# Kernel optimization log

Measured on AMD Instinct MI355X. Metric: run time of the kernel, lower is better.

## Reference

```python
import jax, jax.numpy as jnp
import numpy as np
import math


def setup_inputs() -> dict:
    key = jax.random.key(0)
    ks = jax.random.split(key, 5)
    B, L, H = 16384, 336, 168
    T = L + H
    T_air = jax.random.normal(ks[0], (B, T), dtype=jnp.float32) * 8.0 + 10.0
    T_obs = T_air + jax.random.normal(ks[1], (B, T), dtype=jnp.float32) * 2.0
    wind = jax.random.uniform(ks[2], (B, T), dtype=jnp.float32) * 10.0
    par = jax.random.uniform(ks[3], (B, T), dtype=jnp.float32) * 500.0
    dt = jax.random.uniform(ks[4], (B, T), dtype=jnp.float32) * 3600.0 + 1800.0
    k_init = 1e-4
    k_raw = jnp.float32(k_init + math.log(-math.expm1(-k_init)))  # softplus inverse
    return {
        "T_obs": T_obs, "T_air": T_air, "wind": wind, "par": par, "dt": dt,
        "L_hist": L,
        "k_raw": k_raw,
        "log_q": jnp.float32(-8.0), "log_r": jnp.float32(-4.0),
        "log_p0": jnp.float32(-2.0), "log_q_scale": jnp.float32(0.0),
        "theta_par_lin": jnp.float32(1e-5), "theta_par_quad": jnp.float32(1e-8),
        "theta_wind_cool": jnp.float32(-1e-5), "theta_sensible": jnp.float32(-1e-6),
        "theta_forced_conv": jnp.float32(-1e-7),
    }


def reference(T_obs, T_air, wind, par, dt, L_hist, k_raw, log_q, log_r, log_p0,
              log_q_scale, theta_par_lin, theta_par_quad, theta_wind_cool,
              theta_sensible, theta_forced_conv):
    B, T_total = T_obs.shape
    L = int(L_hist)
    H = T_total - L

    k = jax.nn.softplus(k_raw)
    q = jnp.exp(log_q)
    q_scale = jnp.exp(log_q_scale)
    R = jnp.exp(log_r)
    P0 = jnp.exp(log_p0)

    def predict(T, P, Ta, w, p, dtt):
        dT = T - Ta
        cl = (theta_par_lin * p + theta_par_quad * p * p + theta_wind_cool * w
              + theta_sensible * dT + theta_forced_conv * w * dT)
        T_pred = jnp.clip(T - k * dT * dtt + cl * dtt, -50.0, 100.0)
        F = jnp.clip(1.0 - k * dtt + (theta_sensible + theta_forced_conv * w) * dtt, -2.0, 2.0)
        P_pred = jnp.clip(F * F * P + q_scale * q * dtt, 1e-10, 1e6)
        return T_pred, P_pred

    def filt_step(carry, xs):
        T, P = carry
        Ta, w, p, dtt, y = xs
        Tp, Pp = predict(T, P, Ta, w, p, dtt)
        S = Pp + R
        K = Pp / S
        T_upd = Tp + K * (y - Tp)
        P_upd = (1.0 - K) ** 2 * Pp + K * K * R
        return (T_upd, P_upd), None

    s0 = T_obs[:, 0]
    P0b = jnp.broadcast_to(P0, (B,)).astype(T_obs.dtype)

    # filtering over t = 1 .. L-1 (forcing from t-1, dt/obs at t)
    filt_xs = (T_air[:, :L - 1].T, wind[:, :L - 1].T, par[:, :L - 1].T,
               jnp.clip(dt[:, 1:L], 1.0, None).T, T_obs[:, 1:L].T)
    (s, P), _ = jax.lax.scan(filt_step, (s0, P0b), filt_xs)

    def fcst_step(carry, xs):
        T, P = carry
        Ta, w, p, dtt = xs
        Tp, Pp = predict(T, P, Ta, w, p, dtt)
        return (Tp, Pp), (Tp, Pp)

    # open-loop forecast over t = L .. L+H-1 (forcing from idx-1)
    fcst_xs = (T_air[:, L - 1:L + H - 1].T, wind[:, L - 1:L + H - 1].T,
               par[:, L - 1:L + H - 1].T, jnp.clip(dt[:, L:], 1.0, None).T)
    _, (T_preds, T_vars) = jax.lax.scan(fcst_step, (s, P), fcst_xs)

    return T_preds.T, T_vars.T  # each [B, H]
```

## Files before the change

### kernel.cpp

```cpp
#include <hip/hip_runtime.h>

namespace {
constexpr int kB = 16384;
constexpr int kL = 336;
constexpr int kH = 168;
constexpr int kT = 504;
constexpr int kW = 16;
constexpr int kNW = 32;
constexpr int kFiltW = 21;
constexpr int kRS = 65;
constexpr int kTile = kW * kRS;
constexpr int kORS = 17;
constexpr int kOTile = 64 * kORS;
constexpr int oA  = 0;
constexpr int oWd = oA  + 2 * kTile;
constexpr int oP  = oWd + 2 * kTile;
constexpr int oD  = oP  + 2 * kTile;
constexpr int oY  = oD  + 2 * kTile;
constexpr int oOT = oY  + 2 * kTile;
constexpr int oOV = oOT + 2 * kOTile;
constexpr int kLdsWords = oOV + 2 * kOTile;
}

__global__ __launch_bounds__(256, 1)
void kf_kernel(const float* __restrict__ g_obs,
               const float* __restrict__ g_air,
               const float* __restrict__ g_wind,
               const float* __restrict__ g_par,
               const float* __restrict__ g_dt,
               const float* __restrict__ s_k_raw,
               const float* __restrict__ s_log_q,
               const float* __restrict__ s_log_r,
               const float* __restrict__ s_log_p0,
               const float* __restrict__ s_log_qs,
               const float* __restrict__ s_th_pl,
               const float* __restrict__ s_th_pq,
               const float* __restrict__ s_th_wc,
               const float* __restrict__ s_th_s,
               const float* __restrict__ s_th_fc,
               float* __restrict__ out)
{
    __shared__ float lds[kLdsWords];
    const int tid  = threadIdx.x;
    const int wid  = tid >> 6;
    const int lane = tid & 63;
    const int r0   = blockIdx.x * 64;

    auto stage = [&](const float* __restrict__ g, int basew, int buf, int wn) {
        const int t0 = wn * kW;
        const int tb = basew + buf * kTile;
#pragma unroll
        for (int kk = 0; kk < 4; ++kk) {
            const int flat = kk * 64 + lane;
            const int row = flat >> 2, q = flat & 3;
            int tq = t0 + q * 4;
            tq = tq > 500 ? 500 : tq;
            const float4 v = *(const float4*)(g + (size_t)(r0 + row) * kT + tq);
            const int wb = tb + row + (q * 4) * kRS;
            lds[wb          ] = v.x;
            lds[wb +     kRS] = v.y;
            lds[wb + 2 * kRS] = v.z;
            lds[wb + 3 * kRS] = v.w;
        }
    };

    float* outT = out;
    float* outV = out + (size_t)kB * kH;

    auto store_out = [&](int wn) {
        const int buf = wn & 1;
        const int h0 = wn * kW - kL;
#pragma unroll
        for (int kk = 0; kk < 4; ++kk) {
            const int flat = kk * 64 + lane;
            const int row = flat >> 2, q = flat & 3;
            const int h = h0 + q * 4;
            if (h + 3 < kH) {
                const int rb = oOT + buf * kOTile + row * kORS + q * 4;
                const int vb = oOV + buf * kOTile + row * kORS + q * 4;
                float4 tv, vv;
                tv.x = lds[rb]; tv.y = lds[rb + 1]; tv.z = lds[rb + 2]; tv.w = lds[rb + 3];
                vv.x = lds[vb]; vv.y = lds[vb + 1]; vv.z = lds[vb + 2]; vv.w = lds[vb + 3];
                *(float4*)(outT + (size_t)(r0 + row) * kH + h) = tv;
                *(float4*)(outV + (size_t)(r0 + row) * kH + h) = vv;
            }
        }
    };

    float kpar = 0, qq = 0, R = 0, P = 0, Tst = 0;
    float th_pl = 0, th_pq = 0, th_wc = 0, th_s = 0, th_fc = 0;
    float aC = 0, wC = 0, pC = 0;

    if (wid == 0) {
        kpar = log1pf(expf(s_k_raw[0]));
        qq   = expf(s_log_q[0]) * expf(s_log_qs[0]);
        R    = expf(s_log_r[0]);
        P    = expf(s_log_p0[0]);
        th_pl = s_th_pl[0]; th_pq = s_th_pq[0]; th_wc = s_th_wc[0];
        th_s  = s_th_s[0];  th_fc = s_th_fc[0];
    } else if (wid == 1) {
        stage(g_air, oA, 0, 0); stage(g_wind, oWd, 0, 0);
    } else if (wid == 2) {
        stage(g_par, oP, 0, 0); stage(g_dt, oD, 0, 0);
    } else {
        stage(g_obs, oY, 0, 0);
    }
    __syncthreads();

    for (int w = 0; w < kNW; ++w) {
        const int buf = w & 1;
        if (wid == 0) {
            const int Ab = oA  + buf * kTile, Wb = oWd + buf * kTile;
            const int Pb = oP  + buf * kTile, Db = oD  + buf * kTile;
            const int Yb = oY  + buf * kTile;
            int trel = 0;
            if (w == 0) {
                Tst = lds[Yb + lane];
                aC = lds[Ab + lane]; wC = lds[Wb + lane]; pC = lds[Pb + lane];
                trel = 1;
            }
            if (w < kFiltW) {
                for (; trel < kW; ++trel) {
                    const float D = lds[Db + trel * kRS + lane];
                    const float Y = lds[Yb + trel * kRS + lane];
                    const float dtt = fmaxf(D, 1.0f);
                    const float dT = Tst - aC;
                    const float gk = fmaf(th_fc, wC, th_s) - kpar;
                    const float base = fmaf(pC, fmaf(th_pq, pC, th_pl), th_wc * wC);
                    const float Tp = fminf(fmaxf(fmaf(fmaf(gk, dT, base), dtt, Tst), -50.0f), 100.0f);
                    const float F = fminf(fmaxf(fmaf(gk, dtt, 1.0f), -2.0f), 2.0f);
                    const float Pp = fminf(fmaxf(fmaf(F * F, P, qq * dtt), 1e-10f), 1e6f);
                    const float Kg = Pp * __builtin_amdgcn_rcpf(Pp + R);
                    Tst = fmaf(Kg, Y - Tp, Tp);
                    const float omk = 1.0f - Kg;
                    P = fmaf(omk * omk, Pp, Kg * Kg * R);
                    aC = lds[Ab + trel * kRS + lane];
                    wC = lds[Wb + trel * kRS + lane];
                    pC = lds[Pb + trel * kRS + lane];
                }
            } else {
                const int tmax = (w == kNW - 1) ? 8 : kW;
                const int ob = oOT + buf * kOTile + lane * kORS;
                const int vb = oOV + buf * kOTile + lane * kORS;
                for (; trel < tmax; ++trel) {
                    const float D = lds[Db + trel * kRS + lane];
                    const float dtt = fmaxf(D, 1.0f);
                    const float dT = Tst - aC;
                    const float gk = fmaf(th_fc, wC, th_s) - kpar;
                    const float base = fmaf(pC, fmaf(th_pq, pC, th_pl), th_wc * wC);
                    Tst = fminf(fmaxf(fmaf(fmaf(gk, dT, base), dtt, Tst), -50.0f), 100.0f);
                    const float F = fminf(fmaxf(fmaf(gk, dtt, 1.0f), -2.0f), 2.0f);
                    P = fminf(fmaxf(fmaf(F * F, P, qq * dtt), 1e-10f), 1e6f);
                    lds[ob + trel] = Tst;
                    lds[vb + trel] = P;
                    aC = lds[Ab + trel * kRS + lane];
                    wC = lds[Wb + trel * kRS + lane];
                    pC = lds[Pb + trel * kRS + lane];
                }
            }
        } else if (wid == 1) {
            if (w + 1 < kNW) { stage(g_air, oA, (w + 1) & 1, w + 1);
                               stage(g_wind, oWd, (w + 1) & 1, w + 1); }
        } else if (wid == 2) {
            if (w + 1 < kNW) { stage(g_par, oP, (w + 1) & 1, w + 1);
                               stage(g_dt, oD, (w + 1) & 1, w + 1); }
        } else {
            if (w + 1 < kFiltW) stage(g_obs, oY, (w + 1) & 1, w + 1);
            if (w - 1 >= kFiltW) store_out(w - 1);
        }
        __syncthreads();
    }
    if (wid == 3) store_out(kNW - 1);
}

extern "C" void kernel_launch(void* const* d_in, const int* in_sizes, int n_in,
                              void* d_out, int out_size, void* d_ws, size_t ws_size,
                              hipStream_t stream) {
    const float* g_obs  = (const float*)d_in[0];
    const float* g_air  = (const float*)d_in[1];
    const float* g_wind = (const float*)d_in[2];
    const float* g_par  = (const float*)d_in[3];
    const float* g_dt   = (const float*)d_in[4];
    const float* k_raw  = (const float*)d_in[6];
    const float* log_q  = (const float*)d_in[7];
    const float* log_r  = (const float*)d_in[8];
    const float* log_p0 = (const float*)d_in[9];
    const float* log_qs = (const float*)d_in[10];
    const float* th_pl  = (const float*)d_in[11];
    const float* th_pq  = (const float*)d_in[12];
    const float* th_wc  = (const float*)d_in[13];
    const float* th_s   = (const float*)d_in[14];
    const float* th_fc  = (const float*)d_in[15];
    float* out = (float*)d_out;

    dim3 grid(kB / 64), block(256);
    hipLaunchKernelGGL(kf_kernel, grid, block, 0, stream,
                       g_obs, g_air, g_wind, g_par, g_dt,
                       k_raw, log_q, log_r, log_p0, log_qs,
                       th_pl, th_pq, th_wc, th_s, th_fc, out);
}
```

Measured before the change: 220.7 us.

## Pre-transpose inputs to time-major fp16 workspace and scan with register pipelining

Adds a pre-pass kernel that transposes the five input streams into time-major, 8-step fp16-packed chunks in workspace. A new single-wave scan kernel then reads one coalesced uint4 per stream per chunk and keeps four chunks of loads in flight in registers, replacing the LDS-staged producer/consumer warps. This aims to hide global load latency in the serial recurrence, at the cost of an extra full read/write pass and reduced input precision from fp16 storage. The old kernel remains as a fallback when workspace is too small.

```diff
diff --git a/kernel.cpp b/kernel.cpp
--- a/kernel.cpp
+++ b/kernel.cpp
@@ -1,10 +1,219 @@
 #include <hip/hip_runtime.h>
+#include <hip/hip_fp16.h>
 
 namespace {
 constexpr int kB = 16384;
 constexpr int kL = 336;
 constexpr int kH = 168;
 constexpr int kT = 504;
+constexpr int kC8 = 63;
+constexpr int kFiltC8 = 42;
+constexpr size_t kStreamU4 = (size_t)kC8 * kB;
+constexpr size_t kWsNeed = (4 * (size_t)kC8 + 42) * (size_t)kB * 16;
+}
+
+__global__ __launch_bounds__(256)
+void xpose_kernel(const float* __restrict__ g_obs,
+                  const float* __restrict__ g_air,
+                  const float* __restrict__ g_wind,
+                  const float* __restrict__ g_par,
+                  const float* __restrict__ g_dt,
+                  uint4* __restrict__ ws4)
+{
+    extern __shared__ float tile[];
+    const int tid = threadIdx.x, wid = tid >> 6, lane = tid & 63;
+    const int r0 = blockIdx.x * 64;
+    const int tb = blockIdx.y;
+    const int s  = blockIdx.z;
+    const float* src = s == 0 ? g_air : s == 1 ? g_wind : s == 2 ? g_par
+                     : s == 3 ? g_dt  : g_obs;
+    uint4* dst = ws4 + (size_t)s * kStreamU4;
+    const int t0 = tb * 248;
+
+#pragma unroll
+    for (int it = 0; it < 16; ++it) {
+        const int r = it * 4 + wid;
+        const float4 v = *(const float4*)(src + (size_t)(r0 + r) * kT + t0 + lane * 4);
+        *(float4*)&tile[r * 260 + lane * 4] = v;
+    }
+    __syncthreads();
+
+    const int cbase = tb * 31;
+#pragma unroll
+    for (int it = 0; it < 8; ++it) {
+        const int cl = it * 4 + wid;
+        const int c8 = cbase + cl;
+        if (s == 4 && c8 >= kFiltC8) continue;
+        const float* rp = &tile[lane * 260 + cl * 8];
+        const float4 f0 = *(const float4*)(rp);
+        const float4 f1 = *(const float4*)(rp + 4);
+        union { __half2 h; unsigned u; } c0, c1, c2, c3;
+        c0.h = __floats2half2_rn(f0.x, f0.y);
+        c1.h = __floats2half2_rn(f0.z, f0.w);
+        c2.h = __floats2half2_rn(f1.x, f1.y);
+        c3.h = __floats2half2_rn(f1.z, f1.w);
+        uint4 u; u.x = c0.u; u.y = c1.u; u.z = c2.u; u.w = c3.u;
+        dst[(size_t)c8 * kB + r0 + lane] = u;
+    }
+}
+
+__device__ inline void up2(unsigned u, float& a, float& b) {
+    union { unsigned u; __half2 h; } cv; cv.u = u;
+    const float2 f = __half22float2(cv.h);
+    a = f.x; b = f.y;
+}
+__device__ inline void up8(uint4 u, float* v) {
+    up2(u.x, v[0], v[1]); up2(u.y, v[2], v[3]);
+    up2(u.z, v[4], v[5]); up2(u.w, v[6], v[7]);
+}
+
+struct Qc { uint4 a, w, p, d, y; };
+
+__global__ __launch_bounds__(64, 1)
+void kf_scan_x(const uint4* __restrict__ X,
+               const float* __restrict__ s_k_raw,
+               const float* __restrict__ s_log_q,
+               const float* __restrict__ s_log_r,
+               const float* __restrict__ s_log_p0,
+               const float* __restrict__ s_log_qs,
+               const float* __restrict__ s_th_pl,
+               const float* __restrict__ s_th_pq,
+               const float* __restrict__ s_th_wc,
+               const float* __restrict__ s_th_s,
+               const float* __restrict__ s_th_fc,
+               float* __restrict__ out)
+{
+    extern __shared__ float lt[];
+    float* ldsT = lt;
+    float* ldsV = lt + 64 * 172;
+    const int lane = threadIdx.x;
+    const int b0 = blockIdx.x * 64;
+
+    const uint4* XA = X;
+    const uint4* XW = X + kStreamU4;
+    const uint4* XP = X + 2 * kStreamU4;
+    const uint4* XD = X + 3 * kStreamU4;
+    const uint4* XY = X + 4 * kStreamU4;
+
+    const float kpar = log1pf(expf(s_k_raw[0]));
+    const float qq   = expf(s_log_q[0]) * expf(s_log_qs[0]);
+    const float R    = expf(s_log_r[0]);
+    float P          = expf(s_log_p0[0]);
+    const float th_pl = s_th_pl[0], th_pq = s_th_pq[0], th_wc = s_th_wc[0];
+    const float th_s  = s_th_s[0],  th_fc = s_th_fc[0];
+
+    float Tst = 0.0f, aC = 0.0f, wC = 0.0f, pC = 0.0f;
+
+    auto load = [&](Qc& q, int c) {
+        const int nc = c < kC8 ? c : kC8 - 1;
+        const size_t off = (size_t)nc * kB + b0 + lane;
+        q.a = XA[off]; q.w = XW[off]; q.p = XP[off]; q.d = XD[off];
+        const int yc = nc < kFiltC8 ? nc : kFiltC8 - 1;
+        q.y = XY[(size_t)yc * kB + b0 + lane];
+        __builtin_amdgcn_sched_barrier(0);
+    };
+
+    auto kstep = [&](float Ta, float w, float p, float draw, float y) {
+        const float dtt = fmaxf(draw, 1.0f);
+        const float dT = Tst - Ta;
+        const float gk = fmaf(th_fc, w, th_s) - kpar;
+        const float base = fmaf(p, fmaf(th_pq, p, th_pl), th_wc * w);
+        const float Tp = fminf(fmaxf(fmaf(fmaf(gk, dT, base), dtt, Tst), -50.0f), 100.0f);
+        const float F = fminf(fmaxf(fmaf(gk, dtt, 1.0f), -2.0f), 2.0f);
+        const float Pp = fminf(fmaxf(fmaf(F * F, P, qq * dtt), 1e-10f), 1e6f);
+        const float Kg = Pp * __builtin_amdgcn_rcpf(Pp + R);
+        Tst = fmaf(Kg, y - Tp, Tp);
+        const float omk = 1.0f - Kg;
+        P = fmaf(omk * omk, Pp, Kg * Kg * R);
+    };
+    auto fstep = [&](float Ta, float w, float p, float draw) {
+        const float dtt = fmaxf(draw, 1.0f);
+        const float dT = Tst - Ta;
+        const float gk = fmaf(th_fc, w, th_s) - kpar;
+        const float base = fmaf(p, fmaf(th_pq, p, th_pl), th_wc * w);
+        Tst = fminf(fmaxf(fmaf(fmaf(gk, dT, base), dtt, Tst), -50.0f), 100.0f);
+        const float F = fminf(fmaxf(fmaf(gk, dtt, 1.0f), -2.0f), 2.0f);
+        P = fminf(fmaxf(fmaf(F * F, P, qq * dtt), 1e-10f), 1e6f);
+    };
+
+    auto cK = [&](const Qc& q) {
+        float A[8], W[8], Pr[8], D[8], Y[8];
+        up8(q.a, A); up8(q.w, W); up8(q.p, Pr); up8(q.d, D); up8(q.y, Y);
+        kstep(aC, wC, pC, D[0], Y[0]);
+#pragma unroll
+        for (int j = 1; j < 8; ++j) kstep(A[j-1], W[j-1], Pr[j-1], D[j], Y[j]);
+        aC = A[7]; wC = W[7]; pC = Pr[7];
+    };
+
+    auto cF = [&](const Qc& q, int c) {
+        float A[8], W[8], Pr[8], D[8], oT[8], oV[8];
+        up8(q.a, A); up8(q.w, W); up8(q.p, Pr); up8(q.d, D);
+        fstep(aC, wC, pC, D[0]); oT[0] = Tst; oV[0] = P;
+#pragma unroll
+        for (int j = 1; j < 8; ++j) {
+            fstep(A[j-1], W[j-1], Pr[j-1], D[j]);
+            oT[j] = Tst; oV[j] = P;
+        }
+        aC = A[7]; wC = W[7]; pC = Pr[7];
+        const int h0 = (c - kFiltC8) * 8;
+        *(float4*)&ldsT[lane * 172 + h0    ] = make_float4(oT[0], oT[1], oT[2], oT[3]);
+        *(float4*)&ldsT[lane * 172 + h0 + 4] = make_float4(oT[4], oT[5], oT[6], oT[7]);
+        *(float4*)&ldsV[lane * 172 + h0    ] = make_float4(oV[0], oV[1], oV[2], oV[3]);
+        *(float4*)&ldsV[lane * 172 + h0 + 4] = make_float4(oV[4], oV[5], oV[6], oV[7]);
+    };
+
+    Qc q0, q1, q2, q3;
+    load(q0, 0); load(q1, 1); load(q2, 2); load(q3, 3);
+
+    {
+        float A[8], W[8], Pr[8], D[8], Y[8];
+        up8(q0.a, A); up8(q0.w, W); up8(q0.p, Pr); up8(q0.d, D); up8(q0.y, Y);
+        Tst = Y[0];
+        aC = A[0]; wC = W[0]; pC = Pr[0];
+#pragma unroll
+        for (int j = 1; j < 8; ++j) kstep(A[j-1], W[j-1], Pr[j-1], D[j], Y[j]);
+        aC = A[7]; wC = W[7]; pC = Pr[7];
+    }
+    load(q0, 4);
+    cK(q1); load(q1, 5);
+    cK(q2); load(q2, 6);
+    cK(q3); load(q3, 7);
+
+#pragma unroll 1
+    for (int g = 0; g < 9; ++g) {
+        const int base = 4 * g + 4;
+        cK(q0); load(q0, base + 4);
+        cK(q1); load(q1, base + 5);
+        cK(q2); load(q2, base + 6);
+        cK(q3); load(q3, base + 7);
+    }
+    cK(q0); load(q0, 44);
+    cK(q1); load(q1, 45);
+
+#pragma unroll 1
+    for (int g = 0; g < 5; ++g) {
+        const int base = kFiltC8 + 4 * g;
+        cF(q2, base + 0); load(q2, base + 4);
+        cF(q3, base + 1); load(q3, base + 5);
+        cF(q0, base + 2); load(q0, base + 6);
+        cF(q1, base + 3); load(q1, base + 7);
+    }
+    cF(q2, 62);
+
+    float* outT = out;
+    float* outV = out + (size_t)kB * kH;
+#pragma unroll 1
+    for (int r = 0; r < 64; ++r) {
+        if (lane < 42) {
+            const float4 tv = *(const float4*)&ldsT[r * 172 + lane * 4];
+            const float4 vv = *(const float4*)&ldsV[r * 172 + lane * 4];
+            *(float4*)(outT + (size_t)(b0 + r) * kH + lane * 4) = tv;
+            *(float4*)(outV + (size_t)(b0 + r) * kH + lane * 4) = vv;
+        }
+    }
+}
+
+namespace fb {
 constexpr int kW = 16;
 constexpr int kNW = 32;
 constexpr int kFiltW = 21;
@@ -40,6 +249,7 @@
                const float* __restrict__ s_th_fc,
                float* __restrict__ out)
 {
+    using namespace fb;
     __shared__ float lds[kLdsWords];
     const int tid  = threadIdx.x;
     const int wid  = tid >> 6;
@@ -193,9 +403,21 @@
     const float* th_fc  = (const float*)d_in[15];
     float* out = (float*)d_out;
 
-    dim3 grid(kB / 64), block(256);
-    hipLaunchKernelGGL(kf_kernel, grid, block, 0, stream,
-                       g_obs, g_air, g_wind, g_par, g_dt,
-                       k_raw, log_q, log_r, log_p0, log_qs,
-                       th_pl, th_pq, th_wc, th_s, th_fc, out);
-}
+    if (ws_size >= kWsNeed) {
+        uint4* ws4 = (uint4*)d_ws;
+        dim3 xg(kB / 64, 2, 5), xb(256);
+        hipLaunchKernelGGL(xpose_kernel, xg, xb, 64 * 260 * 4, stream,
+                           g_obs, g_air, g_wind, g_par, g_dt, ws4);
+        dim3 sg(kB / 64), sb(64);
+        hipLaunchKernelGGL(kf_scan_x, sg, sb, 2 * 64 * 172 * 4, stream,
+                           (const uint4*)ws4,
+                           k_raw, log_q, log_r, log_p0, log_qs,
+                           th_pl, th_pq, th_wc, th_s, th_fc, out);
+    } else {
+        dim3 grid(kB / 64), block(256);
+        hipLaunchKernelGGL(kf_kernel, grid, block, 0, stream,
+                           g_obs, g_air, g_wind, g_par, g_dt,
+                           k_raw, log_q, log_r, log_p0, log_qs,
+                           th_pl, th_pq, th_wc, th_s, th_fc, out);
+    }
+}
```

New measurement: 246.5 us. +11.7%, slower.

## Replace block barriers with LDS flag producer-consumer sync and fp16 input staging

Applied to the files above, without the earlier changes.

Removes the per-window __syncthreads that forces the compute wave to wait on loader waves. Loader and compute waves now hand off double-buffered tiles through atomic counters in LDS with sleep-polling. Inputs (air, wind, par, dt, obs) are also converted to fp16 in LDS to halve LDS footprint and traffic. Global loads change from float4 row chunks to scalar loads. The fp16 conversion loses precision: dt up to 5400 and par up to 500 have coarse fp16 spacing, which risks tolerance failures. The polling loop breaks out after a bounded number of spins, which risks a silent race.

```diff
diff --git a/kernel.cpp b/kernel.cpp
--- a/kernel.cpp
+++ b/kernel.cpp
@@ -1,4 +1,5 @@
 #include <hip/hip_runtime.h>
+#include <hip/hip_fp16.h>
 
 namespace {
 constexpr int kB = 16384;
@@ -7,170 +8,198 @@
 constexpr int kT = 504;
 constexpr int kW = 16;
 constexpr int kNW = 32;
-constexpr int kFiltW = 21;
-constexpr int kRS = 65;
-constexpr int kTile = kW * kRS;
-constexpr int kORS = 17;
-constexpr int kOTile = 64 * kORS;
-constexpr int oA  = 0;
-constexpr int oWd = oA  + 2 * kTile;
-constexpr int oP  = oWd + 2 * kTile;
-constexpr int oD  = oP  + 2 * kTile;
-constexpr int oY  = oD  + 2 * kTile;
-constexpr int oOT = oY  + 2 * kTile;
-constexpr int oOV = oOT + 2 * kOTile;
-constexpr int kLdsWords = oOV + 2 * kOTile;
+constexpr int kFW = 21;
+constexpr int kIS = 66;
+constexpr int kITile = kW * kIS;
+constexpr int kOS = 17;
+constexpr int kOTile = 64 * kOS;
+}
+
+__device__ inline void fwait(int* f, int target) {
+    int guard = 0;
+    while (__hip_atomic_load(f, __ATOMIC_ACQUIRE, __HIP_MEMORY_SCOPE_WORKGROUP) < target) {
+        __builtin_amdgcn_s_sleep(1);
+        if (++guard > (1 << 22)) break;
+    }
+}
+__device__ inline void fpost(int* f, int lane) {
+    __threadfence_block();
+    if (lane == 0) atomicAdd(f, 1);
 }
 
 __global__ __launch_bounds__(256, 1)
-void kf_kernel(const float* __restrict__ g_obs,
-               const float* __restrict__ g_air,
-               const float* __restrict__ g_wind,
-               const float* __restrict__ g_par,
-               const float* __restrict__ g_dt,
-               const float* __restrict__ s_k_raw,
-               const float* __restrict__ s_log_q,
-               const float* __restrict__ s_log_r,
-               const float* __restrict__ s_log_p0,
-               const float* __restrict__ s_log_qs,
-               const float* __restrict__ s_th_pl,
-               const float* __restrict__ s_th_pq,
-               const float* __restrict__ s_th_wc,
-               const float* __restrict__ s_th_s,
-               const float* __restrict__ s_th_fc,
-               float* __restrict__ out)
+void kf_fused(const float* __restrict__ g_obs,
+              const float* __restrict__ g_air,
+              const float* __restrict__ g_wind,
+              const float* __restrict__ g_par,
+              const float* __restrict__ g_dt,
+              const float* __restrict__ s_k_raw,
+              const float* __restrict__ s_log_q,
+              const float* __restrict__ s_log_r,
+              const float* __restrict__ s_log_p0,
+              const float* __restrict__ s_log_qs,
+              const float* __restrict__ s_th_pl,
+              const float* __restrict__ s_th_pq,
+              const float* __restrict__ s_th_wc,
+              const float* __restrict__ s_th_s,
+              const float* __restrict__ s_th_fc,
+              float* __restrict__ out)
 {
-    __shared__ float lds[kLdsWords];
-    const int tid  = threadIdx.x;
-    const int wid  = tid >> 6;
-    const int lane = tid & 63;
-    const int r0   = blockIdx.x * 64;
-
-    auto stage = [&](const float* __restrict__ g, int basew, int buf, int wn) {
-        const int t0 = wn * kW;
-        const int tb = basew + buf * kTile;
-#pragma unroll
-        for (int kk = 0; kk < 4; ++kk) {
-            const int flat = kk * 64 + lane;
-            const int row = flat >> 2, q = flat & 3;
-            int tq = t0 + q * 4;
-            tq = tq > 500 ? 500 : tq;
-            const float4 v = *(const float4*)(g + (size_t)(r0 + row) * kT + tq);
-            const int wb = tb + row + (q * 4) * kRS;
-            lds[wb          ] = v.x;
-            lds[wb +     kRS] = v.y;
-            lds[wb + 2 * kRS] = v.z;
-            lds[wb + 3 * kRS] = v.w;
-        }
-    };
-
-    float* outT = out;
-    float* outV = out + (size_t)kB * kH;
-
-    auto store_out = [&](int wn) {
-        const int buf = wn & 1;
-        const int h0 = wn * kW - kL;
-#pragma unroll
-        for (int kk = 0; kk < 4; ++kk) {
-            const int flat = kk * 64 + lane;
-            const int row = flat >> 2, q = flat & 3;
-            const int h = h0 + q * 4;
-            if (h + 3 < kH) {
-                const int rb = oOT + buf * kOTile + row * kORS + q * 4;
-                const int vb = oOV + buf * kOTile + row * kORS + q * 4;
-                float4 tv, vv;
-                tv.x = lds[rb]; tv.y = lds[rb + 1]; tv.z = lds[rb + 2]; tv.w = lds[rb + 3];
-                vv.x = lds[vb]; vv.y = lds[vb + 1]; vv.z = lds[vb + 2]; vv.w = lds[vb + 3];
-                *(float4*)(outT + (size_t)(r0 + row) * kH + h) = tv;
-                *(float4*)(outV + (size_t)(r0 + row) * kH + h) = vv;
-            }
-        }
-    };
-
-    float kpar = 0, qq = 0, R = 0, P = 0, Tst = 0;
-    float th_pl = 0, th_pq = 0, th_wc = 0, th_s = 0, th_fc = 0;
-    float aC = 0, wC = 0, pC = 0;
-
-    if (wid == 0) {
-        kpar = log1pf(expf(s_k_raw[0]));
-        qq   = expf(s_log_q[0]) * expf(s_log_qs[0]);
-        R    = expf(s_log_r[0]);
-        P    = expf(s_log_p0[0]);
-        th_pl = s_th_pl[0]; th_pq = s_th_pq[0]; th_wc = s_th_wc[0];
-        th_s  = s_th_s[0];  th_fc = s_th_fc[0];
-    } else if (wid == 1) {
-        stage(g_air, oA, 0, 0); stage(g_wind, oWd, 0, 0);
-    } else if (wid == 2) {
-        stage(g_par, oP, 0, 0); stage(g_dt, oD, 0, 0);
+    __shared__ __half s_in[5][2][kITile];
+    __shared__ float  s_oT[2][kOTile];
+    __shared__ float  s_oV[2][kOTile];
+    __shared__ int    s_flag[8];
+
+    const int tid = threadIdx.x, wid = tid >> 6, lane = tid & 63;
+    const int b0 = blockIdx.x * 64;
+
+    if (tid < 8) s_flag[tid] = 0;
+    __syncthreads();
+
+    int* pcAW = &s_flag[0];
+    int* pcPD = &s_flag[1];
+    int* pcY  = &s_flag[2];
+    int* cc   = &s_flag[3];
+    int* sc   = &s_flag[4];
+
+    if (wid == 1 || wid == 2) {
+        const float* g0 = (wid == 1) ? g_air  : g_par;
+        const float* g1 = (wid == 1) ? g_wind : g_dt;
+        __half* base0 = (wid == 1) ? &s_in[0][0][0] : &s_in[2][0][0];
+        __half* base1 = (wid == 1) ? &s_in[1][0][0] : &s_in[3][0][0];
+        int* pc = (wid == 1) ? pcAW : pcPD;
+        const int rloc = lane >> 4, trel = lane & 15;
+        for (int w = 0; w < kNW; ++w) {
+            if (w >= 2) fwait(cc, w - 1);
+            const int bi = w & 1;
+            int t = w * kW + trel; if (t > kT - 1) t = kT - 1;
+            float v0[16], v1[16];
+#pragma unroll
+            for (int i = 0; i < 16; ++i) {
+                const size_t off = (size_t)(b0 + 4 * i + rloc) * kT + t;
+                v0[i] = g0[off];
+                v1[i] = g1[off];
+            }
+            __half* d0 = base0 + bi * kITile;
+            __half* d1 = base1 + bi * kITile;
+#pragma unroll
+            for (int i = 0; i < 16; ++i) {
+                const int idx = trel * kIS + 4 * i + rloc;
+                d0[idx] = __float2half(v0[i]);
+                d1[idx] = __float2half(v1[i]);
+            }
+            fpost(pc, lane);
+        }
+    } else if (wid == 3) {
+        const int rloc = lane >> 4, trel = lane & 15;
+        for (int w = 0; w < kFW; ++w) {
+            if (w >= 2) fwait(cc, w - 1);
+            const int bi = w & 1;
+            const int t = w * kW + trel;
+            float v[16];
+#pragma unroll
+            for (int i = 0; i < 16; ++i)
+                v[i] = g_obs[(size_t)(b0 + 4 * i + rloc) * kT + t];
+            __half* d = &s_in[4][bi][0];
+#pragma unroll
+            for (int i = 0; i < 16; ++i)
+                d[trel * kIS + 4 * i + rloc] = __float2half(v[i]);
+            fpost(pcY, lane);
+        }
+        const int rq = lane & 3, rr = lane >> 2;
+        float* outT = out;
+        float* outV = out + (size_t)kB * kH;
+        for (int w = kFW; w < kNW; ++w) {
+            fwait(cc, w + 1);
+            const int bi = w & 1;
+            const int h0 = (w - kFW) * kW;
+            const int nq = (w == kNW - 1) ? 2 : 4;
+#pragma unroll
+            for (int i = 0; i < 4; ++i) {
+                const int r = 16 * i + rr;
+                if (rq < nq) {
+                    const float4 tv = *(const float4*)&s_oT[bi][r * kOS + rq * 4];
+                    const float4 vv = *(const float4*)&s_oV[bi][r * kOS + rq * 4];
+                    *(float4*)&outT[(size_t)(b0 + r) * kH + h0 + rq * 4] = tv;
+                    *(float4*)&outV[(size_t)(b0 + r) * kH + h0 + rq * 4] = vv;
+                }
+            }
+            fpost(sc, lane);
+        }
     } else {
-        stage(g_obs, oY, 0, 0);
-    }
-    __syncthreads();
-
-    for (int w = 0; w < kNW; ++w) {
-        const int buf = w & 1;
-        if (wid == 0) {
-            const int Ab = oA  + buf * kTile, Wb = oWd + buf * kTile;
-            const int Pb = oP  + buf * kTile, Db = oD  + buf * kTile;
-            const int Yb = oY  + buf * kTile;
-            int trel = 0;
-            if (w == 0) {
-                Tst = lds[Yb + lane];
-                aC = lds[Ab + lane]; wC = lds[Wb + lane]; pC = lds[Pb + lane];
-                trel = 1;
-            }
-            if (w < kFiltW) {
+        const float kpar = log1pf(expf(s_k_raw[0]));
+        const float qq   = expf(s_log_q[0]) * expf(s_log_qs[0]);
+        const float R    = expf(s_log_r[0]);
+        float P          = expf(s_log_p0[0]);
+        const float th_pl = s_th_pl[0], th_pq = s_th_pq[0], th_wc = s_th_wc[0];
+        const float th_s  = s_th_s[0],  th_fc = s_th_fc[0];
+        float Tst = 0.0f, aC = 0.0f, wC = 0.0f, pC = 0.0f;
+
+        for (int w = 0; w < kNW; ++w) {
+            const int bi = w & 1;
+            fwait(pcAW, w + 1);
+            fwait(pcPD, w + 1);
+            if (w < kFW) fwait(pcY, w + 1);
+            if (w >= kFW + 2) fwait(sc, w - (kFW + 1));
+
+            const __half* A  = &s_in[0][bi][0];
+            const __half* Wd = &s_in[1][bi][0];
+            const __half* Pr = &s_in[2][bi][0];
+            const __half* Dd = &s_in[3][bi][0];
+            const __half* Yy = &s_in[4][bi][0];
+
+            if (w < kFW) {
+                int trel = 0;
+                if (w == 0) {
+                    Tst = __half2float(Yy[lane]);
+                    aC  = __half2float(A[lane]);
+                    wC  = __half2float(Wd[lane]);
+                    pC  = __half2float(Pr[lane]);
+                    trel = 1;
+                }
                 for (; trel < kW; ++trel) {
-                    const float D = lds[Db + trel * kRS + lane];
-                    const float Y = lds[Yb + trel * kRS + lane];
-                    const float dtt = fmaxf(D, 1.0f);
-                    const float dT = Tst - aC;
-                    const float gk = fmaf(th_fc, wC, th_s) - kpar;
+                    const int ix = trel * kIS + lane;
+                    const float dtt = fmaxf(__half2float(Dd[ix]), 1.0f);
+                    const float y   = __half2float(Yy[ix]);
+                    const float a   = __half2float(A[ix]);
+                    const float wv  = __half2float(Wd[ix]);
+                    const float pv  = __half2float(Pr[ix]);
+                    const float dT  = Tst - aC;
+                    const float gk  = fmaf(th_fc, wC, th_s) - kpar;
                     const float base = fmaf(pC, fmaf(th_pq, pC, th_pl), th_wc * wC);
                     const float Tp = fminf(fmaxf(fmaf(fmaf(gk, dT, base), dtt, Tst), -50.0f), 100.0f);
-                    const float F = fminf(fmaxf(fmaf(gk, dtt, 1.0f), -2.0f), 2.0f);
+                    const float F  = fminf(fmaxf(fmaf(gk, dtt, 1.0f), -2.0f), 2.0f);
                     const float Pp = fminf(fmaxf(fmaf(F * F, P, qq * dtt), 1e-10f), 1e6f);
                     const float Kg = Pp * __builtin_amdgcn_rcpf(Pp + R);
-                    Tst = fmaf(Kg, Y - Tp, Tp);
+                    Tst = fmaf(Kg, y - Tp, Tp);
                     const float omk = 1.0f - Kg;
                     P = fmaf(omk * omk, Pp, Kg * Kg * R);
-                    aC = lds[Ab + trel * kRS + lane];
-                    wC = lds[Wb + trel * kRS + lane];
-                    pC = lds[Pb + trel * kRS + lane];
+                    aC = a; wC = wv; pC = pv;
                 }
             } else {
-                const int tmax = (w == kNW - 1) ? 8 : kW;
-                const int ob = oOT + buf * kOTile + lane * kORS;
-                const int vb = oOV + buf * kOTile + lane * kORS;
-                for (; trel < tmax; ++trel) {
-                    const float D = lds[Db + trel * kRS + lane];
-                    const float dtt = fmaxf(D, 1.0f);
-                    const float dT = Tst - aC;
-                    const float gk = fmaf(th_fc, wC, th_s) - kpar;
+                float* oT = &s_oT[bi][lane * kOS];
+                float* oV = &s_oV[bi][lane * kOS];
+#pragma unroll
+                for (int trel = 0; trel < kW; ++trel) {
+                    const int ix = trel * kIS + lane;
+                    const float dtt = fmaxf(__half2float(Dd[ix]), 1.0f);
+                    const float a   = __half2float(A[ix]);
+                    const float wv  = __half2float(Wd[ix]);
+                    const float pv  = __half2float(Pr[ix]);
+                    const float dT  = Tst - aC;
+                    const float gk  = fmaf(th_fc, wC, th_s) - kpar;
                     const float base = fmaf(pC, fmaf(th_pq, pC, th_pl), th_wc * wC);
                     Tst = fminf(fmaxf(fmaf(fmaf(gk, dT, base), dtt, Tst), -50.0f), 100.0f);
                     const float F = fminf(fmaxf(fmaf(gk, dtt, 1.0f), -2.0f), 2.0f);
                     P = fminf(fmaxf(fmaf(F * F, P, qq * dtt), 1e-10f), 1e6f);
-                    lds[ob + trel] = Tst;
-                    lds[vb + trel] = P;
-                    aC = lds[Ab + trel * kRS + lane];
-                    wC = lds[Wb + trel * kRS + lane];
-                    pC = lds[Pb + trel * kRS + lane];
-                }
-            }
-        } else if (wid == 1) {
-            if (w + 1 < kNW) { stage(g_air, oA, (w + 1) & 1, w + 1);
-                               stage(g_wind, oWd, (w + 1) & 1, w + 1); }
-        } else if (wid == 2) {
-            if (w + 1 < kNW) { stage(g_par, oP, (w + 1) & 1, w + 1);
-                               stage(g_dt, oD, (w + 1) & 1, w + 1); }
-        } else {
-            if (w + 1 < kFiltW) stage(g_obs, oY, (w + 1) & 1, w + 1);
-            if (w - 1 >= kFiltW) store_out(w - 1);
-        }
-        __syncthreads();
+                    oT[trel] = Tst;
+                    oV[trel] = P;
+                    aC = a; wC = wv; pC = pv;
+                }
+            }
+            fpost(cc, lane);
+        }
     }
-    if (wid == 3) store_out(kNW - 1);
 }
 
 extern "C" void kernel_launch(void* const* d_in, const int* in_sizes, int n_in,
@@ -194,7 +223,7 @@
     float* out = (float*)d_out;
 
     dim3 grid(kB / 64), block(256);
-    hipLaunchKernelGGL(kf_kernel, grid, block, 0, stream,
+    hipLaunchKernelGGL(kf_fused, grid, block, 0, stream,
                        g_obs, g_air, g_wind, g_par, g_dt,
                        k_raw, log_q, log_r, log_p0, log_qs,
                        th_pl, th_pq, th_wc, th_s, th_fc, out);
```

After: 220.5 us. About the same (-0.1%).
